# Performance work log

Measured on AMD Instinct MI355X. Metric: run time of the kernel, lower is better.

Reference implementation:

```python
import jax, jax.numpy as jnp
import numpy as np

SOS_TOKEN = 0
VOCAB, EMBED, HIDDEN = 32000, 256, 256


def setup_inputs() -> dict:
    key = jax.random.key(0)
    ks = jax.random.split(key, 10)
    B, S, T = 32, 128, 128
    s = 0.05
    return {
        "encoder_outputs": jax.random.normal(ks[0], (B, S, HIDDEN), jnp.float32),
        "encoder_hidden": jax.random.normal(ks[1], (1, B, HIDDEN), jnp.float32),
        "target_tensor": jax.random.randint(ks[2], (B, T), 0, VOCAB),
        "embedding": jax.random.normal(ks[3], (VOCAB, EMBED), jnp.float32) * s,
        "W_ih": jax.random.normal(ks[4], (3 * HIDDEN, EMBED + HIDDEN), jnp.float32) * s,
        "W_hh": jax.random.normal(ks[5], (3 * HIDDEN, HIDDEN), jnp.float32) * s,
        "b_ih": jax.random.normal(ks[6], (3 * HIDDEN,), jnp.float32) * s,
        "b_hh": jax.random.normal(ks[7], (3 * HIDDEN,), jnp.float32) * s,
        "W_out": jax.random.normal(ks[8], (VOCAB, HIDDEN), jnp.float32) * s,
        "b_out": jax.random.normal(ks[9], (VOCAB,), jnp.float32) * s,
    }


def _decode(encoder_outputs, encoder_hidden, target_tensor, embedding,
            W_ih, W_hh, b_ih, b_hh, W_out, b_out):
    B, T = target_tensor.shape
    # full teacher forcing: decoder input at step t is target[t-1], step 0 is SOS
    dec_in = jnp.concatenate(
        [jnp.full((B, 1), SOS_TOKEN, dtype=target_tensor.dtype), target_tensor[:, :-1]], axis=1)
    emb = embedding[dec_in]                                     # (B,T,E)
    # attention: query = embedded input, key = value = encoder_outputs
    scores = jnp.einsum("bte,bse->bts", emb, encoder_outputs)   # (B,T,S)
    attn = jax.nn.softmax(scores, axis=2)
    context = jnp.einsum("bts,bsh->bth", attn, encoder_outputs)  # (B,T,H)
    x_seq = jnp.concatenate([emb, context], axis=2)             # (B,T,E+H)
    x_seq = jnp.swapaxes(x_seq, 0, 1)                           # (T,B,E+H)

    def gru_step(h, x):
        gi = x @ W_ih.T + b_ih                                  # (B,3H)
        gh = h @ W_hh.T + b_hh
        i_r, i_z, i_n = jnp.split(gi, 3, axis=1)
        h_r, h_z, h_n = jnp.split(gh, 3, axis=1)
        r = jax.nn.sigmoid(i_r + h_r)
        z = jax.nn.sigmoid(i_z + h_z)
        n = jnp.tanh(i_n + r * h_n)
        h_new = (1.0 - z) * n + z * h
        return h_new, h_new

    h0 = encoder_hidden[0]                                      # (B,H)
    _, hs = jax.lax.scan(gru_step, h0, x_seq)                   # (T,B,H)
    logits = hs @ W_out.T + b_out                               # (T,B,V)
    return jnp.swapaxes(logits, 0, 1)                           # (B,T,V)


def reference(encoder_outputs, encoder_hidden, target_tensor, embedding,
              W_ih, W_hh, b_ih, b_hh, W_out, b_out):
    return _decode(encoder_outputs, encoder_hidden, target_tensor, embedding,
                   W_ih, W_hh, b_ih, b_hh, W_out, b_out)
```

## Files before the change

kernel.cpp:

```cpp
#include <hip/hip_runtime.h>
#include <hip/hip_bf16.h>
#include <stdint.h>

typedef float    f32x4  __attribute__((ext_vector_type(4)));
typedef __bf16   bf16x8 __attribute__((ext_vector_type(8)));
typedef _Float16 f16x8  __attribute__((ext_vector_type(8)));
typedef _Float16 h2v    __attribute__((ext_vector_type(2)));

#define B_ 32
#define S_ 128
#define T_ 128
#define H_ 256
#define E_ 256
#define V_ 32000

__device__ __forceinline__ void gll16(const void* g, void* l) {
  __builtin_amdgcn_global_load_lds(
      (const __attribute__((address_space(1))) uint32_t*)g,
      (__attribute__((address_space(3))) uint32_t*)l,
      16, 0, 0);
}

__device__ __forceinline__ uint32_t pack_pair(float a, float b) {
  unsigned short lo = __builtin_bit_cast(unsigned short, (_Float16)a);
  unsigned short hi = __builtin_bit_cast(unsigned short, (_Float16)b);
  return (uint32_t)lo | ((uint32_t)hi << 16);
}

__device__ __forceinline__ float dot2(uint32_t w, uint32_t h, float acc) {
#if __has_builtin(__builtin_amdgcn_fdot2)
  return __builtin_amdgcn_fdot2(__builtin_bit_cast(h2v, w),
                                __builtin_bit_cast(h2v, h), acc, false);
#else
  h2v wv = __builtin_bit_cast(h2v, w);
  h2v hv = __builtin_bit_cast(h2v, h);
  return acc + (float)wv.x * (float)hv.x + (float)wv.y * (float)hv.y;
#endif
}

__device__ __forceinline__ float sigmoid_fast(float x) {
  return __fdividef(1.f, 1.f + __expf(-x));
}
__device__ __forceinline__ float tanh_fast(float x) {
  float e = __expf(2.f * fabsf(x));
  float t = 1.f - __fdividef(2.f, e + 1.f);
  return copysignf(t, x);
}

__global__ __launch_bounds__(256) void cvt_bf16_kernel(
    const float* __restrict__ src, uint32_t* __restrict__ dst, int n) {
  int i = (blockIdx.x * 256 + threadIdx.x) * 8;
  if (i + 7 < n) {
    float4 a = *(const float4*)(src + i);
    float4 b = *(const float4*)(src + i + 4);
    uint4 o;
    o.x = (uint32_t)__builtin_bit_cast(unsigned short, __float2bfloat16(a.x)) |
          ((uint32_t)__builtin_bit_cast(unsigned short, __float2bfloat16(a.y)) << 16);
    o.y = (uint32_t)__builtin_bit_cast(unsigned short, __float2bfloat16(a.z)) |
          ((uint32_t)__builtin_bit_cast(unsigned short, __float2bfloat16(a.w)) << 16);
    o.z = (uint32_t)__builtin_bit_cast(unsigned short, __float2bfloat16(b.x)) |
          ((uint32_t)__builtin_bit_cast(unsigned short, __float2bfloat16(b.y)) << 16);
    o.w = (uint32_t)__builtin_bit_cast(unsigned short, __float2bfloat16(b.z)) |
          ((uint32_t)__builtin_bit_cast(unsigned short, __float2bfloat16(b.w)) << 16);
    *(uint4*)(dst + (i >> 1)) = o;
  }
}

__global__ __launch_bounds__(256) void cvt_f16_kernel(
    const float* __restrict__ src, uint32_t* __restrict__ dst, int n) {
  int i = (blockIdx.x * 256 + threadIdx.x) * 4;
  if (i + 3 < n) {
    float4 v = *(const float4*)(src + i);
    uint2 p;
    p.x = pack_pair(v.x, v.y);
    p.y = pack_pair(v.z, v.w);
    *(uint2*)(dst + (i >> 1)) = p;
  }
}

__global__ __launch_bounds__(256) void pack_whh(
    const float* __restrict__ Whh, uint32_t* __restrict__ Wp) {
  __shared__ float lds[32][257];
  int j0 = blockIdx.x * 32;
  int tid = threadIdx.x;
  #pragma unroll 4
  for (int i = 0; i < 32; ++i)
    lds[i][tid] = Whh[(size_t)(j0 + i) * 256 + tid];
  __syncthreads();
  #pragma unroll 4
  for (int i = 0; i < 16; ++i) {
    int e = i * 256 + tid;
    int k2 = e >> 5;
    int jj = e & 31;
    Wp[(size_t)k2 * 768 + j0 + jj] = pack_pair(lds[jj][2 * k2], lds[jj][2 * k2 + 1]);
  }
}

__global__ __launch_bounds__(256) void attn_kernel(
    const float* __restrict__ enc,
    const int*   __restrict__ tgt,
    const float* __restrict__ embt,
    uint32_t*    __restrict__ xh)
{
  int b   = blockIdx.x;
  int tc  = blockIdx.y;
  int tid = threadIdx.x;
  __shared__ __align__(16) float e_sh[256];
  __shared__ float attn_sh[128];
  __shared__ float red_sh[4];
  const float* encb = enc + (size_t)b * S_ * H_;

  for (int tt = 0; tt < 8; ++tt) {
    int t = tc * 8 + tt;
    int tok = (t == 0) ? 0 : tgt[b * T_ + t - 1];
    float ev = embt[(size_t)tok * E_ + tid];
    e_sh[tid] = ev;
    {
      float other = __shfl_xor(ev, 1);
      if (!(tid & 1))
        xh[(size_t)(t * B_ + b) * 256 + (tid >> 1)] = pack_pair(ev, other);
    }
    __syncthreads();

    float sc = 0.f;
    if (tid < 128) {
      const float* er = encb + tid * H_;
      #pragma unroll 8
      for (int k = 0; k < 256; k += 4) {
        float4 e4 = *(const float4*)(e_sh + k);
        float4 r4 = *(const float4*)(er + k);
        sc += e4.x * r4.x; sc += e4.y * r4.y; sc += e4.z * r4.z; sc += e4.w * r4.w;
      }
      float mx = sc;
      #pragma unroll
      for (int o = 32; o > 0; o >>= 1) mx = fmaxf(mx, __shfl_xor(mx, o, 64));
      if ((tid & 63) == 0) red_sh[tid >> 6] = mx;
    }
    __syncthreads();
    float gmax = fmaxf(red_sh[0], red_sh[1]);
    float p = 0.f;
    if (tid < 128) {
      p = __expf(sc - gmax);
      float s = p;
      #pragma unroll
      for (int o = 32; o > 0; o >>= 1) s += __shfl_xor(s, o, 64);
      if ((tid & 63) == 0) red_sh[2 + (tid >> 6)] = s;
    }
    __syncthreads();
    float tot = red_sh[2] + red_sh[3];
    if (tid < 128) attn_sh[tid] = p / tot;
    __syncthreads();

    float ctx = 0.f;
    #pragma unroll 4
    for (int s = 0; s < 128; ++s) ctx += attn_sh[s] * encb[s * H_ + tid];
    {
      float other = __shfl_xor(ctx, 1);
      if (!(tid & 1))
        xh[(size_t)(t * B_ + b) * 256 + 128 + (tid >> 1)] = pack_pair(ctx, other);
    }
    __syncthreads();
  }
}

__global__ __launch_bounds__(256) void gi_gemm_f16(
    const _Float16* __restrict__ A,
    const _Float16* __restrict__ Bm,
    const float* __restrict__ bih,
    float* __restrict__ gi)
{
  __shared__ _Float16 sA[128 * 64];
  __shared__ _Float16 sB[128 * 64];
  int tid = threadIdx.x;
  int n0 = blockIdx.x * 128;
  int m0 = blockIdx.y * 128;
  int lane = tid & 63;
  int wave = tid >> 6;
  int wm = (wave >> 1) * 64;
  int wn = (wave & 1) * 64;
  int srow = tid >> 3;
  int sk   = (tid & 7) * 8;
  f32x4 acc[4][4] = {};

  for (int kt = 0; kt < 512; kt += 64) {
    #pragma unroll
    for (int it = 0; it < 4; ++it) {
      int row = it * 32 + srow;
      gll16(A  + (size_t)(m0 + row) * 512 + kt + sk, &sA[row * 64 + sk]);
      gll16(Bm + (size_t)(n0 + row) * 512 + kt + sk, &sB[row * 64 + sk]);
    }
    __syncthreads();
    #pragma unroll
    for (int kk = 0; kk < 2; ++kk) {
      f16x8 af[4], bfr[4];
      #pragma unroll
      for (int m = 0; m < 4; ++m)
        af[m] = *(const f16x8*)&sA[(wm + m * 16 + (lane & 15)) * 64 + kk * 32 + (lane >> 4) * 8];
      #pragma unroll
      for (int n = 0; n < 4; ++n)
        bfr[n] = *(const f16x8*)&sB[(wn + n * 16 + (lane & 15)) * 64 + kk * 32 + (lane >> 4) * 8];
      #pragma unroll
      for (int m = 0; m < 4; ++m)
        #pragma unroll
        for (int n = 0; n < 4; ++n)
          acc[m][n] = __builtin_amdgcn_mfma_f32_16x16x32_f16(af[m], bfr[n], acc[m][n], 0, 0, 0);
    }
    __syncthreads();
  }

  #pragma unroll
  for (int n = 0; n < 4; ++n) {
    int col = n0 + wn + n * 16 + (lane & 15);
    float bv = bih[col];
    #pragma unroll
    for (int m = 0; m < 4; ++m) {
      int rbase = m0 + wm + m * 16 + (lane >> 4) * 4;
      #pragma unroll
      for (int r = 0; r < 4; ++r)
        gi[(size_t)(rbase + r) * 768 + col] = acc[m][n][r] + bv;
    }
  }
}

__global__ __launch_bounds__(768) void gru_kernel(
    const float*    __restrict__ gi,
    const uint32_t* __restrict__ Wp,
    const float*    __restrict__ bhh,
    const float*    __restrict__ h0,
    __hip_bfloat16* __restrict__ hs)
{
  int b   = blockIdx.x;
  int tid = threadIdx.x;
  int role = tid >> 8;
  int j    = tid & 255;
  __shared__ __align__(16) uint32_t h2[128];
  __shared__ float r_sh[256];
  __shared__ float z_sh[256];

  uint32_t w[128];
  #pragma unroll
  for (int i = 0; i < 128; ++i) w[i] = Wp[(size_t)i * 768 + tid];
  float bj = bhh[tid];

  float hprev = 0.f;
  if (role == 2) {
    hprev = h0[b * 256 + j];
    float other = __shfl_xor(hprev, 1);
    if (!(j & 1)) h2[j >> 1] = pack_pair(hprev, other);
  }
  float gval = gi[(size_t)b * 768 + tid];
  __syncthreads();

  for (int t = 0; t < 128; ++t) {
    float gnext = 0.f;
    if (t < 127) gnext = gi[(size_t)((t + 1) * 32 + b) * 768 + tid];

    float a0 = 0.f, a1 = 0.f, a2 = 0.f, a3 = 0.f;
    float a4 = 0.f, a5 = 0.f, a6 = 0.f, a7 = 0.f;
    #pragma unroll
    for (int k8 = 0; k8 < 16; ++k8) {
      uint4 ha = *(const uint4*)&h2[k8 * 8];
      uint4 hb = *(const uint4*)&h2[k8 * 8 + 4];
      a0 = dot2(w[k8 * 8 + 0], ha.x, a0);
      a1 = dot2(w[k8 * 8 + 1], ha.y, a1);
      a2 = dot2(w[k8 * 8 + 2], ha.z, a2);
      a3 = dot2(w[k8 * 8 + 3], ha.w, a3);
      a4 = dot2(w[k8 * 8 + 4], hb.x, a4);
      a5 = dot2(w[k8 * 8 + 5], hb.y, a5);
      a6 = dot2(w[k8 * 8 + 6], hb.z, a6);
      a7 = dot2(w[k8 * 8 + 7], hb.w, a7);
    }
    float gh = ((a0 + a1) + (a2 + a3)) + ((a4 + a5) + (a6 + a7)) + bj;

    if (role == 0)      r_sh[j] = sigmoid_fast(gval + gh);
    else if (role == 1) z_sh[j] = sigmoid_fast(gval + gh);
    __syncthreads();

    if (role == 2) {
      float r = r_sh[j];
      float z = z_sh[j];
      float n = tanh_fast(gval + r * gh);
      float hn = (1.f - z) * n + z * hprev;
      hprev = hn;
      hs[(size_t)(t * 32 + b) * 256 + j] = __float2bfloat16(hn);
      float other = __shfl_xor(hn, 1);
      if (!(j & 1)) h2[j >> 1] = pack_pair(hn, other);
    }
    gval = gnext;
    __syncthreads();
  }
}

__global__ __launch_bounds__(256) void logits_gemm(
    const __hip_bfloat16* __restrict__ A,
    const __hip_bfloat16* __restrict__ Bm,
    const float* __restrict__ bout,
    float* __restrict__ out)
{
  __shared__ __hip_bfloat16 sA[128 * 64];
  __shared__ __hip_bfloat16 sB[128 * 64];
  int tid = threadIdx.x;
  int bid = blockIdx.x;
  int chunk = bid & 7;
  int local = bid >> 3;
  int m0 = (chunk * 4 + (local & 3)) * 128;
  int n0 = (local >> 2) * 128;
  int lane = tid & 63;
  int wave = tid >> 6;
  int wm = (wave >> 1) * 64;
  int wn = (wave & 1) * 64;
  int srow = tid >> 3;
  int sk   = (tid & 7) * 8;
  f32x4 acc[4][4] = {};

  for (int kt = 0; kt < 256; kt += 64) {
    #pragma unroll
    for (int it = 0; it < 4; ++it) {
      int row = it * 32 + srow;
      gll16(A  + (size_t)(m0 + row) * 256 + kt + sk, &sA[row * 64 + sk]);
      gll16(Bm + (size_t)(n0 + row) * 256 + kt + sk, &sB[row * 64 + sk]);
    }
    __syncthreads();
    #pragma unroll
    for (int kk = 0; kk < 2; ++kk) {
      bf16x8 af[4], bfr[4];
      #pragma unroll
      for (int m = 0; m < 4; ++m)
        af[m] = *(const bf16x8*)&sA[(wm + m * 16 + (lane & 15)) * 64 + kk * 32 + (lane >> 4) * 8];
      #pragma unroll
      for (int n = 0; n < 4; ++n)
        bfr[n] = *(const bf16x8*)&sB[(wn + n * 16 + (lane & 15)) * 64 + kk * 32 + (lane >> 4) * 8];
      #pragma unroll
      for (int m = 0; m < 4; ++m)
        #pragma unroll
        for (int n = 0; n < 4; ++n)
          acc[m][n] = __builtin_amdgcn_mfma_f32_16x16x32_bf16(af[m], bfr[n], acc[m][n], 0, 0, 0);
    }
    __syncthreads();
  }

  #pragma unroll
  for (int n = 0; n < 4; ++n) {
    int col = n0 + wn + n * 16 + (lane & 15);
    float bv = bout[col];
    #pragma unroll
    for (int m = 0; m < 4; ++m) {
      int rbase = m0 + wm + m * 16 + (lane >> 4) * 4;
      #pragma unroll
      for (int r = 0; r < 4; ++r) {
        int row = rbase + r;
        int t  = row >> 5;
        int bb = row & 31;
        out[(size_t)(bb * 128 + t) * 32000 + col] = acc[m][n][r] + bv;
      }
    }
  }
}

extern "C" void kernel_launch(void* const* d_in, const int* in_sizes, int n_in,
                              void* d_out, int out_size, void* d_ws, size_t ws_size,
                              hipStream_t stream) {
  const float* enc  = (const float*)d_in[0];
  const float* ench = (const float*)d_in[1];
  const int*   tgt  = (const int*)d_in[2];
  const float* embt = (const float*)d_in[3];
  const float* Wih  = (const float*)d_in[4];
  const float* Whh  = (const float*)d_in[5];
  const float* bih  = (const float*)d_in[6];
  const float* bhh  = (const float*)d_in[7];
  const float* Wout = (const float*)d_in[8];
  const float* bout = (const float*)d_in[9];
  float* out = (float*)d_out;

  char* ws = (char*)d_ws;
  float*          gi    = (float*)(ws);
  __hip_bfloat16* hs    = (__hip_bfloat16*)(ws + 12582912);
  __hip_bfloat16* woutb = (__hip_bfloat16*)(ws + 14680064);
  uint32_t*       xh    = (uint32_t*)(ws + 31064064);
  uint32_t*       wihh  = (uint32_t*)(ws + 35258368);

  uint32_t* Wp = (uint32_t*)(out + ((size_t)out_size - 98304));

  cvt_bf16_kernel<<<4000, 256, 0, stream>>>(Wout, (uint32_t*)woutb, V_ * H_);
  cvt_f16_kernel<<<384, 256, 0, stream>>>(Wih, wihh, 768 * 512);
  pack_whh<<<24, 256, 0, stream>>>(Whh, Wp);
  attn_kernel<<<dim3(32, 16), 256, 0, stream>>>(enc, tgt, embt, xh);
  gi_gemm_f16<<<dim3(6, 32), 256, 0, stream>>>((const _Float16*)xh, (const _Float16*)wihh, bih, gi);
  gru_kernel<<<32, 768, 0, stream>>>(gi, Wp, bhh, ench, hs);
  logits_gemm<<<8000, 256, 0, stream>>>(hs, woutb, bout, out);
}
```

Measured before the change: 482.9 us.

## Merge prep kernels into one launch and halve GRU threads with split reg/LDS weights

Folds the four preprocessing kernels (W_out bf16 convert, W_ih f16 convert, W_hh pack, attention) into a single prep_kernel launch dispatched by block index, removing three launch gaps. The GRU kernel now uses 384 threads that each compute two gate columns. Each thread keeps 112 of its 128 packed-weight pairs in registers and reads the remaining 16 rows from a 48KB LDS copy of W_hh. The goal is fewer waves contending per step on the serial recurrence, at the cost of higher register pressure (risk of spills) and extra LDS reads per step.

```diff
diff --git a/kernel.cpp b/kernel.cpp
--- a/kernel.cpp
+++ b/kernel.cpp
@@ -13,6 +13,8 @@
 #define H_ 256
 #define E_ 256
 #define V_ 32000
+#define REG_K8 14
+#define LDS_K2 16
 
 __device__ __forceinline__ void gll16(const void* g, void* l) {
   __builtin_amdgcn_global_load_lds(
@@ -25,6 +27,11 @@
   unsigned short lo = __builtin_bit_cast(unsigned short, (_Float16)a);
   unsigned short hi = __builtin_bit_cast(unsigned short, (_Float16)b);
   return (uint32_t)lo | ((uint32_t)hi << 16);
+}
+
+__device__ __forceinline__ uint32_t pack_bf16(float a, float b) {
+  return (uint32_t)__builtin_bit_cast(unsigned short, __float2bfloat16(a)) |
+         ((uint32_t)__builtin_bit_cast(unsigned short, __float2bfloat16(b)) << 16);
 }
 
 __device__ __forceinline__ float dot2(uint32_t w, uint32_t h, float acc) {
@@ -47,119 +54,122 @@
   return copysignf(t, x);
 }
 
-__global__ __launch_bounds__(256) void cvt_bf16_kernel(
-    const float* __restrict__ src, uint32_t* __restrict__ dst, int n) {
-  int i = (blockIdx.x * 256 + threadIdx.x) * 8;
-  if (i + 7 < n) {
-    float4 a = *(const float4*)(src + i);
-    float4 b = *(const float4*)(src + i + 4);
+#define GRU_DOT8(W0,W1,W2,W3,W4,W5,W6,W7,HA,HB)                     \
+  a0 = dot2((W0).x,(HA).x,a0); b0 = dot2((W0).y,(HA).x,b0);         \
+  a1 = dot2((W1).x,(HA).y,a1); b1 = dot2((W1).y,(HA).y,b1);         \
+  a2 = dot2((W2).x,(HA).z,a2); b2 = dot2((W2).y,(HA).z,b2);         \
+  a3 = dot2((W3).x,(HA).w,a3); b3 = dot2((W3).y,(HA).w,b3);         \
+  a0 = dot2((W4).x,(HB).x,a0); b0 = dot2((W4).y,(HB).x,b0);         \
+  a1 = dot2((W5).x,(HB).y,a1); b1 = dot2((W5).y,(HB).y,b1);         \
+  a2 = dot2((W6).x,(HB).z,a2); b2 = dot2((W6).y,(HB).z,b2);         \
+  a3 = dot2((W7).x,(HB).w,a3); b3 = dot2((W7).y,(HB).w,b3);
+
+__global__ __launch_bounds__(256) void prep_kernel(
+    const float* __restrict__ Wout, uint32_t* __restrict__ woutb,
+    const float* __restrict__ Wih,  uint32_t* __restrict__ wihh,
+    const float* __restrict__ Whh,  uint32_t* __restrict__ Wp,
+    const float* __restrict__ enc, const int* __restrict__ tgt,
+    const float* __restrict__ embt, uint32_t* __restrict__ xh)
+{
+  __shared__ __align__(16) char smem[32896];
+  int bid = blockIdx.x;
+  int tid = threadIdx.x;
+
+  if (bid < 4000) {
+    int i = (bid * 256 + tid) * 8;
+    float4 a = *(const float4*)(Wout + i);
+    float4 b = *(const float4*)(Wout + i + 4);
     uint4 o;
-    o.x = (uint32_t)__builtin_bit_cast(unsigned short, __float2bfloat16(a.x)) |
-          ((uint32_t)__builtin_bit_cast(unsigned short, __float2bfloat16(a.y)) << 16);
-    o.y = (uint32_t)__builtin_bit_cast(unsigned short, __float2bfloat16(a.z)) |
-          ((uint32_t)__builtin_bit_cast(unsigned short, __float2bfloat16(a.w)) << 16);
-    o.z = (uint32_t)__builtin_bit_cast(unsigned short, __float2bfloat16(b.x)) |
-          ((uint32_t)__builtin_bit_cast(unsigned short, __float2bfloat16(b.y)) << 16);
-    o.w = (uint32_t)__builtin_bit_cast(unsigned short, __float2bfloat16(b.z)) |
-          ((uint32_t)__builtin_bit_cast(unsigned short, __float2bfloat16(b.w)) << 16);
-    *(uint4*)(dst + (i >> 1)) = o;
-  }
-}
-
-__global__ __launch_bounds__(256) void cvt_f16_kernel(
-    const float* __restrict__ src, uint32_t* __restrict__ dst, int n) {
-  int i = (blockIdx.x * 256 + threadIdx.x) * 4;
-  if (i + 3 < n) {
-    float4 v = *(const float4*)(src + i);
+    o.x = pack_bf16(a.x, a.y); o.y = pack_bf16(a.z, a.w);
+    o.z = pack_bf16(b.x, b.y); o.w = pack_bf16(b.z, b.w);
+    *(uint4*)(woutb + (i >> 1)) = o;
+    return;
+  }
+  if (bid < 4384) {
+    int i = ((bid - 4000) * 256 + tid) * 4;
+    float4 v = *(const float4*)(Wih + i);
     uint2 p;
     p.x = pack_pair(v.x, v.y);
     p.y = pack_pair(v.z, v.w);
-    *(uint2*)(dst + (i >> 1)) = p;
-  }
-}
-
-__global__ __launch_bounds__(256) void pack_whh(
-    const float* __restrict__ Whh, uint32_t* __restrict__ Wp) {
-  __shared__ float lds[32][257];
-  int j0 = blockIdx.x * 32;
-  int tid = threadIdx.x;
-  #pragma unroll 4
-  for (int i = 0; i < 32; ++i)
-    lds[i][tid] = Whh[(size_t)(j0 + i) * 256 + tid];
-  __syncthreads();
-  #pragma unroll 4
-  for (int i = 0; i < 16; ++i) {
-    int e = i * 256 + tid;
-    int k2 = e >> 5;
-    int jj = e & 31;
-    Wp[(size_t)k2 * 768 + j0 + jj] = pack_pair(lds[jj][2 * k2], lds[jj][2 * k2 + 1]);
-  }
-}
-
-__global__ __launch_bounds__(256) void attn_kernel(
-    const float* __restrict__ enc,
-    const int*   __restrict__ tgt,
-    const float* __restrict__ embt,
-    uint32_t*    __restrict__ xh)
-{
-  int b   = blockIdx.x;
-  int tc  = blockIdx.y;
-  int tid = threadIdx.x;
-  __shared__ __align__(16) float e_sh[256];
-  __shared__ float attn_sh[128];
-  __shared__ float red_sh[4];
-  const float* encb = enc + (size_t)b * S_ * H_;
-
-  for (int tt = 0; tt < 8; ++tt) {
-    int t = tc * 8 + tt;
-    int tok = (t == 0) ? 0 : tgt[b * T_ + t - 1];
-    float ev = embt[(size_t)tok * E_ + tid];
-    e_sh[tid] = ev;
-    {
-      float other = __shfl_xor(ev, 1);
-      if (!(tid & 1))
-        xh[(size_t)(t * B_ + b) * 256 + (tid >> 1)] = pack_pair(ev, other);
-    }
-    __syncthreads();
-
-    float sc = 0.f;
-    if (tid < 128) {
-      const float* er = encb + tid * H_;
-      #pragma unroll 8
-      for (int k = 0; k < 256; k += 4) {
-        float4 e4 = *(const float4*)(e_sh + k);
-        float4 r4 = *(const float4*)(er + k);
-        sc += e4.x * r4.x; sc += e4.y * r4.y; sc += e4.z * r4.z; sc += e4.w * r4.w;
+    *(uint2*)(wihh + (i >> 1)) = p;
+    return;
+  }
+  if (bid < 4408) {
+    float (*lds)[257] = (float(*)[257])smem;
+    int j0 = (bid - 4384) * 32;
+    #pragma unroll 4
+    for (int i = 0; i < 32; ++i)
+      lds[i][tid] = Whh[(size_t)(j0 + i) * 256 + tid];
+    __syncthreads();
+    #pragma unroll 4
+    for (int i = 0; i < 16; ++i) {
+      int e = i * 256 + tid;
+      int k2 = e >> 5;
+      int jj = e & 31;
+      Wp[(size_t)k2 * 768 + j0 + jj] = pack_pair(lds[jj][2 * k2], lds[jj][2 * k2 + 1]);
+    }
+    return;
+  }
+  {
+    int idx = bid - 4408;
+    int b   = idx & 31;
+    int tc  = idx >> 5;
+    float* e_sh    = (float*)smem;
+    float* attn_sh = e_sh + 256;
+    float* red_sh  = attn_sh + 128;
+    const float* encb = enc + (size_t)b * S_ * H_;
+
+    for (int tt = 0; tt < 8; ++tt) {
+      int t = tc * 8 + tt;
+      int tok = (t == 0) ? 0 : tgt[b * T_ + t - 1];
+      float ev = embt[(size_t)tok * E_ + tid];
+      e_sh[tid] = ev;
+      {
+        float other = __shfl_xor(ev, 1);
+        if (!(tid & 1))
+          xh[(size_t)(t * B_ + b) * 256 + (tid >> 1)] = pack_pair(ev, other);
       }
-      float mx = sc;
-      #pragma unroll
-      for (int o = 32; o > 0; o >>= 1) mx = fmaxf(mx, __shfl_xor(mx, o, 64));
-      if ((tid & 63) == 0) red_sh[tid >> 6] = mx;
-    }
-    __syncthreads();
-    float gmax = fmaxf(red_sh[0], red_sh[1]);
-    float p = 0.f;
-    if (tid < 128) {
-      p = __expf(sc - gmax);
-      float s = p;
-      #pragma unroll
-      for (int o = 32; o > 0; o >>= 1) s += __shfl_xor(s, o, 64);
-      if ((tid & 63) == 0) red_sh[2 + (tid >> 6)] = s;
-    }
-    __syncthreads();
-    float tot = red_sh[2] + red_sh[3];
-    if (tid < 128) attn_sh[tid] = p / tot;
-    __syncthreads();
-
-    float ctx = 0.f;
-    #pragma unroll 4
-    for (int s = 0; s < 128; ++s) ctx += attn_sh[s] * encb[s * H_ + tid];
-    {
-      float other = __shfl_xor(ctx, 1);
-      if (!(tid & 1))
-        xh[(size_t)(t * B_ + b) * 256 + 128 + (tid >> 1)] = pack_pair(ctx, other);
-    }
-    __syncthreads();
+      __syncthreads();
+
+      float sc = 0.f;
+      if (tid < 128) {
+        const float* er = encb + tid * H_;
+        #pragma unroll 8
+        for (int k = 0; k < 256; k += 4) {
+          float4 e4 = *(const float4*)(e_sh + k);
+          float4 r4 = *(const float4*)(er + k);
+          sc += e4.x * r4.x; sc += e4.y * r4.y; sc += e4.z * r4.z; sc += e4.w * r4.w;
+        }
+        float mx = sc;
+        #pragma unroll
+        for (int o = 32; o > 0; o >>= 1) mx = fmaxf(mx, __shfl_xor(mx, o, 64));
+        if ((tid & 63) == 0) red_sh[tid >> 6] = mx;
+      }
+      __syncthreads();
+      float gmax = fmaxf(red_sh[0], red_sh[1]);
+      float p = 0.f;
+      if (tid < 128) {
+        p = __expf(sc - gmax);
+        float s = p;
+        #pragma unroll
+        for (int o = 32; o > 0; o >>= 1) s += __shfl_xor(s, o, 64);
+        if ((tid & 63) == 0) red_sh[2 + (tid >> 6)] = s;
+      }
+      __syncthreads();
+      float tot = red_sh[2] + red_sh[3];
+      if (tid < 128) attn_sh[tid] = p / tot;
+      __syncthreads();
+
+      float ctx = 0.f;
+      #pragma unroll 4
+      for (int s = 0; s < 128; ++s) ctx += attn_sh[s] * encb[s * H_ + tid];
+      {
+        float other = __shfl_xor(ctx, 1);
+        if (!(tid & 1))
+          xh[(size_t)(t * B_ + b) * 256 + 128 + (tid >> 1)] = pack_pair(ctx, other);
+      }
+      __syncthreads();
+    }
   }
 }
 
@@ -222,71 +232,93 @@
   }
 }
 
-__global__ __launch_bounds__(768) void gru_kernel(
+__global__ __launch_bounds__(384, 1) void gru_kernel(
     const float*    __restrict__ gi,
     const uint32_t* __restrict__ Wp,
     const float*    __restrict__ bhh,
     const float*    __restrict__ h0,
     __hip_bfloat16* __restrict__ hs)
 {
-  int b   = blockIdx.x;
-  int tid = threadIdx.x;
-  int role = tid >> 8;
-  int j    = tid & 255;
+  int bb  = blockIdx.x;
+  int t0  = threadIdx.x;
+  int c0  = 2 * t0;
+  int role = t0 >> 7;
+  int d   = (t0 - 256) * 2;
+
   __shared__ __align__(16) uint32_t h2[128];
   __shared__ float r_sh[256];
   __shared__ float z_sh[256];
-
-  uint32_t w[128];
+  __shared__ uint32_t wl[LDS_K2 * 768];
+
+  uint2 w[REG_K8 * 8];
   #pragma unroll
-  for (int i = 0; i < 128; ++i) w[i] = Wp[(size_t)i * 768 + tid];
-  float bj = bhh[tid];
-
-  float hprev = 0.f;
+  for (int i = 0; i < REG_K8 * 8; ++i)
+    w[i] = *(const uint2*)&Wp[(size_t)i * 768 + c0];
+  for (int i = t0; i < LDS_K2 * 768; i += 384)
+    wl[i] = Wp[(size_t)112 * 768 + i];
+
+  float bj0 = bhh[c0], bj1 = bhh[c0 + 1];
+
+  float2 hp = {0.f, 0.f};
   if (role == 2) {
-    hprev = h0[b * 256 + j];
-    float other = __shfl_xor(hprev, 1);
-    if (!(j & 1)) h2[j >> 1] = pack_pair(hprev, other);
-  }
-  float gval = gi[(size_t)b * 768 + tid];
+    hp = *(const float2*)&h0[bb * 256 + d];
+    h2[t0 - 256] = pack_pair(hp.x, hp.y);
+  }
+  float2 g = *(const float2*)&gi[(size_t)bb * 768 + c0];
   __syncthreads();
 
   for (int t = 0; t < 128; ++t) {
-    float gnext = 0.f;
-    if (t < 127) gnext = gi[(size_t)((t + 1) * 32 + b) * 768 + tid];
+    float2 gn2 = {0.f, 0.f};
+    if (t < 127) gn2 = *(const float2*)&gi[(size_t)((t + 1) * 32 + bb) * 768 + c0];
 
     float a0 = 0.f, a1 = 0.f, a2 = 0.f, a3 = 0.f;
-    float a4 = 0.f, a5 = 0.f, a6 = 0.f, a7 = 0.f;
-    #pragma unroll
-    for (int k8 = 0; k8 < 16; ++k8) {
+    float b0 = 0.f, b1 = 0.f, b2 = 0.f, b3 = 0.f;
+    #pragma unroll
+    for (int k8 = 0; k8 < REG_K8; ++k8) {
       uint4 ha = *(const uint4*)&h2[k8 * 8];
       uint4 hb = *(const uint4*)&h2[k8 * 8 + 4];
-      a0 = dot2(w[k8 * 8 + 0], ha.x, a0);
-      a1 = dot2(w[k8 * 8 + 1], ha.y, a1);
-      a2 = dot2(w[k8 * 8 + 2], ha.z, a2);
-      a3 = dot2(w[k8 * 8 + 3], ha.w, a3);
-      a4 = dot2(w[k8 * 8 + 4], hb.x, a4);
-      a5 = dot2(w[k8 * 8 + 5], hb.y, a5);
-      a6 = dot2(w[k8 * 8 + 6], hb.z, a6);
-      a7 = dot2(w[k8 * 8 + 7], hb.w, a7);
-    }
-    float gh = ((a0 + a1) + (a2 + a3)) + ((a4 + a5) + (a6 + a7)) + bj;
-
-    if (role == 0)      r_sh[j] = sigmoid_fast(gval + gh);
-    else if (role == 1) z_sh[j] = sigmoid_fast(gval + gh);
+      GRU_DOT8(w[k8*8+0], w[k8*8+1], w[k8*8+2], w[k8*8+3],
+               w[k8*8+4], w[k8*8+5], w[k8*8+6], w[k8*8+7], ha, hb);
+    }
+    #pragma unroll
+    for (int k8 = REG_K8; k8 < 16; ++k8) {
+      uint4 ha = *(const uint4*)&h2[k8 * 8];
+      uint4 hb = *(const uint4*)&h2[k8 * 8 + 4];
+      const uint32_t* wrow = &wl[(k8 - REG_K8) * 8 * 768 + c0];
+      uint2 v0 = *(const uint2*)(wrow + 0 * 768);
+      uint2 v1 = *(const uint2*)(wrow + 1 * 768);
+      uint2 v2 = *(const uint2*)(wrow + 2 * 768);
+      uint2 v3 = *(const uint2*)(wrow + 3 * 768);
+      uint2 v4 = *(const uint2*)(wrow + 4 * 768);
+      uint2 v5 = *(const uint2*)(wrow + 5 * 768);
+      uint2 v6 = *(const uint2*)(wrow + 6 * 768);
+      uint2 v7 = *(const uint2*)(wrow + 7 * 768);
+      GRU_DOT8(v0, v1, v2, v3, v4, v5, v6, v7, ha, hb);
+    }
+    float gh0 = (a0 + a1) + (a2 + a3) + bj0;
+    float gh1 = (b0 + b1) + (b2 + b3) + bj1;
+
+    if (role == 0) {
+      float2 rr = {sigmoid_fast(g.x + gh0), sigmoid_fast(g.y + gh1)};
+      *(float2*)&r_sh[c0] = rr;
+    } else if (role == 1) {
+      float2 zz = {sigmoid_fast(g.x + gh0), sigmoid_fast(g.y + gh1)};
+      *(float2*)&z_sh[c0 - 256] = zz;
+    }
     __syncthreads();
 
     if (role == 2) {
-      float r = r_sh[j];
-      float z = z_sh[j];
-      float n = tanh_fast(gval + r * gh);
-      float hn = (1.f - z) * n + z * hprev;
-      hprev = hn;
-      hs[(size_t)(t * 32 + b) * 256 + j] = __float2bfloat16(hn);
-      float other = __shfl_xor(hn, 1);
-      if (!(j & 1)) h2[j >> 1] = pack_pair(hn, other);
-    }
-    gval = gnext;
+      float2 rr = *(const float2*)&r_sh[d];
+      float2 zz = *(const float2*)&z_sh[d];
+      float n0 = tanh_fast(g.x + rr.x * gh0);
+      float n1 = tanh_fast(g.y + rr.y * gh1);
+      float hn0 = (1.f - zz.x) * n0 + zz.x * hp.x;
+      float hn1 = (1.f - zz.y) * n1 + zz.y * hp.y;
+      hp = {hn0, hn1};
+      *(uint32_t*)&hs[(size_t)(t * 32 + bb) * 256 + d] = pack_bf16(hn0, hn1);
+      h2[t0 - 256] = pack_pair(hn0, hn1);
+    }
+    g = gn2;
     __syncthreads();
   }
 }
@@ -381,11 +413,9 @@
 
   uint32_t* Wp = (uint32_t*)(out + ((size_t)out_size - 98304));
 
-  cvt_bf16_kernel<<<4000, 256, 0, stream>>>(Wout, (uint32_t*)woutb, V_ * H_);
-  cvt_f16_kernel<<<384, 256, 0, stream>>>(Wih, wihh, 768 * 512);
-  pack_whh<<<24, 256, 0, stream>>>(Whh, Wp);
-  attn_kernel<<<dim3(32, 16), 256, 0, stream>>>(enc, tgt, embt, xh);
+  prep_kernel<<<4920, 256, 0, stream>>>(Wout, (uint32_t*)woutb, Wih, wihh,
+                                        Whh, Wp, enc, tgt, embt, xh);
   gi_gemm_f16<<<dim3(6, 32), 256, 0, stream>>>((const _Float16*)xh, (const _Float16*)wihh, bih, gi);
-  gru_kernel<<<32, 768, 0, stream>>>(gi, Wp, bhh, ench, hs);
+  gru_kernel<<<32, 384, 0, stream>>>(gi, Wp, bhh, ench, hs);
   logits_gemm<<<8000, 256, 0, stream>>>(hs, woutb, bout, out);
 }
```

Result: slower. 623.7 us (+29.2%).

## Merge prep kernels into one launch and widen logits GEMM tile to 128x256

Applied to the files above, without the earlier changes.

The four preprocessing kernels (Wout bf16 conversion, Wih f16 conversion, Whh packing, attention) become a single block-indexed kernel, removing three launches and letting their work overlap on the device. The logits GEMM moves to 512-thread blocks computing 128x256 tiles, so each A tile loaded into LDS is reused across twice as many output columns and half as many blocks launch. The cost is a larger shared-memory footprint per block, which can lower occupancy, and the attention blocks share an oversized LDS allocation with the other roles.

```diff
diff --git a/kernel.cpp b/kernel.cpp
--- a/kernel.cpp
+++ b/kernel.cpp
@@ -25,6 +25,11 @@
   unsigned short lo = __builtin_bit_cast(unsigned short, (_Float16)a);
   unsigned short hi = __builtin_bit_cast(unsigned short, (_Float16)b);
   return (uint32_t)lo | ((uint32_t)hi << 16);
+}
+
+__device__ __forceinline__ uint32_t pack_bf16(float a, float b) {
+  return (uint32_t)__builtin_bit_cast(unsigned short, __float2bfloat16(a)) |
+         ((uint32_t)__builtin_bit_cast(unsigned short, __float2bfloat16(b)) << 16);
 }
 
 __device__ __forceinline__ float dot2(uint32_t w, uint32_t h, float acc) {
@@ -47,119 +52,112 @@
   return copysignf(t, x);
 }
 
-__global__ __launch_bounds__(256) void cvt_bf16_kernel(
-    const float* __restrict__ src, uint32_t* __restrict__ dst, int n) {
-  int i = (blockIdx.x * 256 + threadIdx.x) * 8;
-  if (i + 7 < n) {
-    float4 a = *(const float4*)(src + i);
-    float4 b = *(const float4*)(src + i + 4);
+__global__ __launch_bounds__(256) void prep_kernel(
+    const float* __restrict__ Wout, uint32_t* __restrict__ woutb,
+    const float* __restrict__ Wih,  uint32_t* __restrict__ wihh,
+    const float* __restrict__ Whh,  uint32_t* __restrict__ Wp,
+    const float* __restrict__ enc, const int* __restrict__ tgt,
+    const float* __restrict__ embt, uint32_t* __restrict__ xh)
+{
+  __shared__ __align__(16) char smem[32896];
+  int bid = blockIdx.x;
+  int tid = threadIdx.x;
+
+  if (bid < 4000) {
+    int i = (bid * 256 + tid) * 8;
+    float4 a = *(const float4*)(Wout + i);
+    float4 b = *(const float4*)(Wout + i + 4);
     uint4 o;
-    o.x = (uint32_t)__builtin_bit_cast(unsigned short, __float2bfloat16(a.x)) |
-          ((uint32_t)__builtin_bit_cast(unsigned short, __float2bfloat16(a.y)) << 16);
-    o.y = (uint32_t)__builtin_bit_cast(unsigned short, __float2bfloat16(a.z)) |
-          ((uint32_t)__builtin_bit_cast(unsigned short, __float2bfloat16(a.w)) << 16);
-    o.z = (uint32_t)__builtin_bit_cast(unsigned short, __float2bfloat16(b.x)) |
-          ((uint32_t)__builtin_bit_cast(unsigned short, __float2bfloat16(b.y)) << 16);
-    o.w = (uint32_t)__builtin_bit_cast(unsigned short, __float2bfloat16(b.z)) |
-          ((uint32_t)__builtin_bit_cast(unsigned short, __float2bfloat16(b.w)) << 16);
-    *(uint4*)(dst + (i >> 1)) = o;
-  }
-}
-
-__global__ __launch_bounds__(256) void cvt_f16_kernel(
-    const float* __restrict__ src, uint32_t* __restrict__ dst, int n) {
-  int i = (blockIdx.x * 256 + threadIdx.x) * 4;
-  if (i + 3 < n) {
-    float4 v = *(const float4*)(src + i);
+    o.x = pack_bf16(a.x, a.y); o.y = pack_bf16(a.z, a.w);
+    o.z = pack_bf16(b.x, b.y); o.w = pack_bf16(b.z, b.w);
+    *(uint4*)(woutb + (i >> 1)) = o;
+    return;
+  }
+  if (bid < 4384) {
+    int i = ((bid - 4000) * 256 + tid) * 4;
+    float4 v = *(const float4*)(Wih + i);
     uint2 p;
     p.x = pack_pair(v.x, v.y);
     p.y = pack_pair(v.z, v.w);
-    *(uint2*)(dst + (i >> 1)) = p;
-  }
-}
-
-__global__ __launch_bounds__(256) void pack_whh(
-    const float* __restrict__ Whh, uint32_t* __restrict__ Wp) {
-  __shared__ float lds[32][257];
-  int j0 = blockIdx.x * 32;
-  int tid = threadIdx.x;
-  #pragma unroll 4
-  for (int i = 0; i < 32; ++i)
-    lds[i][tid] = Whh[(size_t)(j0 + i) * 256 + tid];
-  __syncthreads();
-  #pragma unroll 4
-  for (int i = 0; i < 16; ++i) {
-    int e = i * 256 + tid;
-    int k2 = e >> 5;
-    int jj = e & 31;
-    Wp[(size_t)k2 * 768 + j0 + jj] = pack_pair(lds[jj][2 * k2], lds[jj][2 * k2 + 1]);
-  }
-}
-
-__global__ __launch_bounds__(256) void attn_kernel(
-    const float* __restrict__ enc,
-    const int*   __restrict__ tgt,
-    const float* __restrict__ embt,
-    uint32_t*    __restrict__ xh)
-{
-  int b   = blockIdx.x;
-  int tc  = blockIdx.y;
-  int tid = threadIdx.x;
-  __shared__ __align__(16) float e_sh[256];
-  __shared__ float attn_sh[128];
-  __shared__ float red_sh[4];
-  const float* encb = enc + (size_t)b * S_ * H_;
-
-  for (int tt = 0; tt < 8; ++tt) {
-    int t = tc * 8 + tt;
-    int tok = (t == 0) ? 0 : tgt[b * T_ + t - 1];
-    float ev = embt[(size_t)tok * E_ + tid];
-    e_sh[tid] = ev;
-    {
-      float other = __shfl_xor(ev, 1);
-      if (!(tid & 1))
-        xh[(size_t)(t * B_ + b) * 256 + (tid >> 1)] = pack_pair(ev, other);
-    }
-    __syncthreads();
-
-    float sc = 0.f;
-    if (tid < 128) {
-      const float* er = encb + tid * H_;
-      #pragma unroll 8
-      for (int k = 0; k < 256; k += 4) {
-        float4 e4 = *(const float4*)(e_sh + k);
-        float4 r4 = *(const float4*)(er + k);
-        sc += e4.x * r4.x; sc += e4.y * r4.y; sc += e4.z * r4.z; sc += e4.w * r4.w;
-      }
-      float mx = sc;
-      #pragma unroll
-      for (int o = 32; o > 0; o >>= 1) mx = fmaxf(mx, __shfl_xor(mx, o, 64));
-      if ((tid & 63) == 0) red_sh[tid >> 6] = mx;
-    }
-    __syncthreads();
-    float gmax = fmaxf(red_sh[0], red_sh[1]);
-    float p = 0.f;
-    if (tid < 128) {
-      p = __expf(sc - gmax);
-      float s = p;
-      #pragma unroll
-      for (int o = 32; o > 0; o >>= 1) s += __shfl_xor(s, o, 64);
-      if ((tid & 63) == 0) red_sh[2 + (tid >> 6)] = s;
-    }
-    __syncthreads();
-    float tot = red_sh[2] + red_sh[3];
-    if (tid < 128) attn_sh[tid] = p / tot;
-    __syncthreads();
-
-    float ctx = 0.f;
+    *(uint2*)(wihh + (i >> 1)) = p;
+    return;
+  }
+  if (bid < 4408) {
+    float (*lds)[257] = (float(*)[257])smem;
+    int j0 = (bid - 4384) * 32;
     #pragma unroll 4
-    for (int s = 0; s < 128; ++s) ctx += attn_sh[s] * encb[s * H_ + tid];
-    {
-      float other = __shfl_xor(ctx, 1);
-      if (!(tid & 1))
-        xh[(size_t)(t * B_ + b) * 256 + 128 + (tid >> 1)] = pack_pair(ctx, other);
-    }
-    __syncthreads();
+    for (int i = 0; i < 32; ++i)
+      lds[i][tid] = Whh[(size_t)(j0 + i) * 256 + tid];
+    __syncthreads();
+    #pragma unroll 4
+    for (int i = 0; i < 16; ++i) {
+      int e = i * 256 + tid;
+      int k2 = e >> 5;
+      int jj = e & 31;
+      Wp[(size_t)k2 * 768 + j0 + jj] = pack_pair(lds[jj][2 * k2], lds[jj][2 * k2 + 1]);
+    }
+    return;
+  }
+  {
+    int idx = bid - 4408;
+    int b   = idx & 31;
+    int tc  = idx >> 5;
+    float* e_sh    = (float*)smem;
+    float* attn_sh = e_sh + 256;
+    float* red_sh  = attn_sh + 128;
+    const float* encb = enc + (size_t)b * S_ * H_;
+
+    for (int tt = 0; tt < 8; ++tt) {
+      int t = tc * 8 + tt;
+      int tok = (t == 0) ? 0 : tgt[b * T_ + t - 1];
+      float ev = embt[(size_t)tok * E_ + tid];
+      e_sh[tid] = ev;
+      {
+        float other = __shfl_xor(ev, 1);
+        if (!(tid & 1))
+          xh[(size_t)(t * B_ + b) * 256 + (tid >> 1)] = pack_pair(ev, other);
+      }
+      __syncthreads();
+
+      float sc = 0.f;
+      if (tid < 128) {
+        const float* er = encb + tid * H_;
+        #pragma unroll 8
+        for (int k = 0; k < 256; k += 4) {
+          float4 e4 = *(const float4*)(e_sh + k);
+          float4 r4 = *(const float4*)(er + k);
+          sc += e4.x * r4.x; sc += e4.y * r4.y; sc += e4.z * r4.z; sc += e4.w * r4.w;
+        }
+        float mx = sc;
+        #pragma unroll
+        for (int o = 32; o > 0; o >>= 1) mx = fmaxf(mx, __shfl_xor(mx, o, 64));
+        if ((tid & 63) == 0) red_sh[tid >> 6] = mx;
+      }
+      __syncthreads();
+      float gmax = fmaxf(red_sh[0], red_sh[1]);
+      float p = 0.f;
+      if (tid < 128) {
+        p = __expf(sc - gmax);
+        float s = p;
+        #pragma unroll
+        for (int o = 32; o > 0; o >>= 1) s += __shfl_xor(s, o, 64);
+        if ((tid & 63) == 0) red_sh[2 + (tid >> 6)] = s;
+      }
+      __syncthreads();
+      float tot = red_sh[2] + red_sh[3];
+      if (tid < 128) attn_sh[tid] = p / tot;
+      __syncthreads();
+
+      float ctx = 0.f;
+      #pragma unroll 4
+      for (int s = 0; s < 128; ++s) ctx += attn_sh[s] * encb[s * H_ + tid];
+      {
+        float other = __shfl_xor(ctx, 1);
+        if (!(tid & 1))
+          xh[(size_t)(t * B_ + b) * 256 + 128 + (tid >> 1)] = pack_pair(ctx, other);
+      }
+      __syncthreads();
+    }
   }
 }
 
@@ -291,33 +289,37 @@
   }
 }
 
-__global__ __launch_bounds__(256) void logits_gemm(
+__global__ __launch_bounds__(512) void logits_gemm(
     const __hip_bfloat16* __restrict__ A,
     const __hip_bfloat16* __restrict__ Bm,
     const float* __restrict__ bout,
     float* __restrict__ out)
 {
   __shared__ __hip_bfloat16 sA[128 * 64];
-  __shared__ __hip_bfloat16 sB[128 * 64];
+  __shared__ __hip_bfloat16 sB[256 * 64];
   int tid = threadIdx.x;
   int bid = blockIdx.x;
   int chunk = bid & 7;
   int local = bid >> 3;
   int m0 = (chunk * 4 + (local & 3)) * 128;
-  int n0 = (local >> 2) * 128;
+  int n0 = (local >> 2) * 256;
   int lane = tid & 63;
   int wave = tid >> 6;
-  int wm = (wave >> 1) * 64;
-  int wn = (wave & 1) * 64;
+  int wm = (wave >> 2) * 64;
+  int wn = (wave & 3) * 64;
   int srow = tid >> 3;
   int sk   = (tid & 7) * 8;
   f32x4 acc[4][4] = {};
 
   for (int kt = 0; kt < 256; kt += 64) {
     #pragma unroll
+    for (int it = 0; it < 2; ++it) {
+      int row = it * 64 + srow;
+      gll16(A + (size_t)(m0 + row) * 256 + kt + sk, &sA[row * 64 + sk]);
+    }
+    #pragma unroll
     for (int it = 0; it < 4; ++it) {
-      int row = it * 32 + srow;
-      gll16(A  + (size_t)(m0 + row) * 256 + kt + sk, &sA[row * 64 + sk]);
+      int row = it * 64 + srow;
       gll16(Bm + (size_t)(n0 + row) * 256 + kt + sk, &sB[row * 64 + sk]);
     }
     __syncthreads();
@@ -381,11 +383,9 @@
 
   uint32_t* Wp = (uint32_t*)(out + ((size_t)out_size - 98304));
 
-  cvt_bf16_kernel<<<4000, 256, 0, stream>>>(Wout, (uint32_t*)woutb, V_ * H_);
-  cvt_f16_kernel<<<384, 256, 0, stream>>>(Wih, wihh, 768 * 512);
-  pack_whh<<<24, 256, 0, stream>>>(Whh, Wp);
-  attn_kernel<<<dim3(32, 16), 256, 0, stream>>>(enc, tgt, embt, xh);
+  prep_kernel<<<4920, 256, 0, stream>>>(Wout, (uint32_t*)woutb, Wih, wihh,
+                                        Whh, Wp, enc, tgt, embt, xh);
   gi_gemm_f16<<<dim3(6, 32), 256, 0, stream>>>((const _Float16*)xh, (const _Float16*)wihh, bih, gi);
   gru_kernel<<<32, 768, 0, stream>>>(gi, Wp, bhh, ench, hs);
-  logits_gemm<<<8000, 256, 0, stream>>>(hs, woutb, bout, out);
-}
+  logits_gemm<<<4000, 512, 0, stream>>>(hs, woutb, bout, out);
+}
```

Measured after the change: 526.8 us. 1.09x slower.

## Swizzle LDS tiles and swap MFMA operands for vectorized output stores

Applied to the files above, without the earlier changes.

The output projection GEMM now stores its shared-memory tiles with an XOR swizzle on the 16-byte chunk index, so the fragment reads spread across LDS banks and avoid conflicts. The MFMA operands are also swapped, which leaves each lane holding four consecutive output columns instead of four rows. The epilogue can then write float4 vectors and load the bias as a vector, replacing scattered scalar stores. The large fp32 logits write is meant to get cheaper, at the cost of extra index arithmetic.

```diff
diff --git a/kernel.cpp b/kernel.cpp
--- a/kernel.cpp
+++ b/kernel.cpp
@@ -25,6 +25,11 @@
   unsigned short lo = __builtin_bit_cast(unsigned short, (_Float16)a);
   unsigned short hi = __builtin_bit_cast(unsigned short, (_Float16)b);
   return (uint32_t)lo | ((uint32_t)hi << 16);
+}
+
+__device__ __forceinline__ uint32_t pack_bf16(float a, float b) {
+  return (uint32_t)__builtin_bit_cast(unsigned short, __float2bfloat16(a)) |
+         ((uint32_t)__builtin_bit_cast(unsigned short, __float2bfloat16(b)) << 16);
 }
 
 __device__ __forceinline__ float dot2(uint32_t w, uint32_t h, float acc) {
@@ -54,14 +59,10 @@
     float4 a = *(const float4*)(src + i);
     float4 b = *(const float4*)(src + i + 4);
     uint4 o;
-    o.x = (uint32_t)__builtin_bit_cast(unsigned short, __float2bfloat16(a.x)) |
-          ((uint32_t)__builtin_bit_cast(unsigned short, __float2bfloat16(a.y)) << 16);
-    o.y = (uint32_t)__builtin_bit_cast(unsigned short, __float2bfloat16(a.z)) |
-          ((uint32_t)__builtin_bit_cast(unsigned short, __float2bfloat16(a.w)) << 16);
-    o.z = (uint32_t)__builtin_bit_cast(unsigned short, __float2bfloat16(b.x)) |
-          ((uint32_t)__builtin_bit_cast(unsigned short, __float2bfloat16(b.y)) << 16);
-    o.w = (uint32_t)__builtin_bit_cast(unsigned short, __float2bfloat16(b.z)) |
-          ((uint32_t)__builtin_bit_cast(unsigned short, __float2bfloat16(b.w)) << 16);
+    o.x = pack_bf16(a.x, a.y);
+    o.y = pack_bf16(a.z, a.w);
+    o.z = pack_bf16(b.x, b.y);
+    o.w = pack_bf16(b.z, b.w);
     *(uint4*)(dst + (i >> 1)) = o;
   }
 }
@@ -310,49 +311,53 @@
   int wm = (wave >> 1) * 64;
   int wn = (wave & 1) * 64;
   int srow = tid >> 3;
-  int sk   = (tid & 7) * 8;
+  int schunk = tid & 7;
   f32x4 acc[4][4] = {};
 
   for (int kt = 0; kt < 256; kt += 64) {
     #pragma unroll
     for (int it = 0; it < 4; ++it) {
       int row = it * 32 + srow;
-      gll16(A  + (size_t)(m0 + row) * 256 + kt + sk, &sA[row * 64 + sk]);
-      gll16(Bm + (size_t)(n0 + row) * 256 + kt + sk, &sB[row * 64 + sk]);
+      int gc = ((schunk ^ (row & 7)) * 8);
+      gll16(A  + (size_t)(m0 + row) * 256 + kt + gc, &sA[row * 64 + schunk * 8]);
+      gll16(Bm + (size_t)(n0 + row) * 256 + kt + gc, &sB[row * 64 + schunk * 8]);
     }
     __syncthreads();
     #pragma unroll
     for (int kk = 0; kk < 2; ++kk) {
       bf16x8 af[4], bfr[4];
       #pragma unroll
-      for (int m = 0; m < 4; ++m)
-        af[m] = *(const bf16x8*)&sA[(wm + m * 16 + (lane & 15)) * 64 + kk * 32 + (lane >> 4) * 8];
-      #pragma unroll
-      for (int n = 0; n < 4; ++n)
-        bfr[n] = *(const bf16x8*)&sB[(wn + n * 16 + (lane & 15)) * 64 + kk * 32 + (lane >> 4) * 8];
+      for (int m = 0; m < 4; ++m) {
+        int r = wm + m * 16 + (lane & 15);
+        int pc = ((kk * 4 + (lane >> 4)) ^ (r & 7)) * 8;
+        af[m] = *(const bf16x8*)&sA[r * 64 + pc];
+      }
+      #pragma unroll
+      for (int n = 0; n < 4; ++n) {
+        int r = wn + n * 16 + (lane & 15);
+        int pc = ((kk * 4 + (lane >> 4)) ^ (r & 7)) * 8;
+        bfr[n] = *(const bf16x8*)&sB[r * 64 + pc];
+      }
       #pragma unroll
       for (int m = 0; m < 4; ++m)
         #pragma unroll
         for (int n = 0; n < 4; ++n)
-          acc[m][n] = __builtin_amdgcn_mfma_f32_16x16x32_bf16(af[m], bfr[n], acc[m][n], 0, 0, 0);
+          acc[m][n] = __builtin_amdgcn_mfma_f32_16x16x32_bf16(bfr[n], af[m], acc[m][n], 0, 0, 0);
     }
     __syncthreads();
   }
 
   #pragma unroll
-  for (int n = 0; n < 4; ++n) {
-    int col = n0 + wn + n * 16 + (lane & 15);
-    float bv = bout[col];
-    #pragma unroll
-    for (int m = 0; m < 4; ++m) {
-      int rbase = m0 + wm + m * 16 + (lane >> 4) * 4;
-      #pragma unroll
-      for (int r = 0; r < 4; ++r) {
-        int row = rbase + r;
-        int t  = row >> 5;
-        int bb = row & 31;
-        out[(size_t)(bb * 128 + t) * 32000 + col] = acc[m][n][r] + bv;
-      }
+  for (int m = 0; m < 4; ++m) {
+    int row = m0 + wm + m * 16 + (lane & 15);
+    int t  = row >> 5;
+    int bb = row & 31;
+    float* orow = out + (size_t)(bb * 128 + t) * 32000;
+    #pragma unroll
+    for (int n = 0; n < 4; ++n) {
+      int col0 = n0 + wn + n * 16 + (lane >> 4) * 4;
+      f32x4 bv = *(const f32x4*)&bout[col0];
+      *(f32x4*)&orow[col0] = acc[m][n] + bv;
     }
   }
 }
```

Measured after the change: 488.3 us. Within noise of the previous version (+1.1%).
